# Performance work log

Measured on AMD Instinct MI355X. Metric: run time of the kernel, lower is better.

## Reference

```python
import jax, jax.numpy as jnp
import numpy as np

COUPLE_STRENGTH = 0.1
ITER_FISTA = 16
ITER_EIGENVAL = 20


def setup_inputs() -> dict:
    key = jax.random.key(0)
    k1, k2 = jax.random.split(key)
    # light field patches: (b, N, u, v, s, t, ch)
    x = jax.random.normal(k1, (8, 256, 5, 5, 4, 4, 3), dtype=jnp.float32)
    dim_signal = 5 * 5 * 4 * 4 * 3  # 1200
    dim_dict = 2 * dim_signal       # overcompleteness = 2 -> 2400
    D = jax.random.normal(k2, (dim_signal, dim_dict), dtype=jnp.float32)
    D = D / jnp.linalg.norm(D, axis=0, keepdims=True)  # UnitNorm(axis=0) constraint
    return {"x": x, "dictionary": D}


def _max_eigval(D):
    """von Mises power iteration for largest eigenvalue of D^T D."""
    v0 = jax.random.normal(jax.random.key(42), (D.shape[1],), dtype=D.dtype)
    v0 = v0 / jnp.linalg.norm(v0)

    def step(v, _):
        w = D.T @ (D @ v)
        n = jnp.linalg.norm(w)
        return w / n, n

    _, norms = jax.lax.scan(step, v0, None, length=ITER_EIGENVAL)
    return norms[-1]


def _soft_threshold(x, thr):
    return jnp.sign(x) * jnp.maximum(jnp.abs(x) - thr, 0.0)


def _sparse_code_fista(x2, D):
    """x2: (B, N, dim_signal); D: (dim_signal, dim_dict) -> codes (B, N, dim_dict)."""
    L = _max_eigval(D)            # Lipschitz constant of grad of 0.5*||Dz - x||^2
    thr = COUPLE_STRENGTH / L
    z0 = jnp.zeros(x2.shape[:-1] + (D.shape[1],), dtype=x2.dtype)
    carry0 = (z0, z0, jnp.float32(1.0))  # (z, y, t)

    def step(carry, _):
        z, y, t = carry
        recon = jnp.einsum('bnk,dk->bnd', y, D)             # (B,N,ds)
        grad = jnp.einsum('bnd,dk->bnk', recon - x2, D)     # (B,N,dd)
        z_new = _soft_threshold(y - grad / L, thr)
        t_new = 0.5 * (1.0 + jnp.sqrt(1.0 + 4.0 * t * t))
        y_new = z_new + ((t - 1.0) / t_new) * (z_new - z)   # Nesterov momentum
        return (z_new, y_new, t_new), None

    (z, _, _), _ = jax.lax.scan(step, carry0, None, length=ITER_FISTA)
    return z


def reference(x, dictionary):
    B, N, u, v, s, t, ch = x.shape
    x2 = x.reshape(B, N, u * v * s * t * ch)
    code = jax.lax.stop_gradient(_sparse_code_fista(x2, dictionary))
    recon = jnp.einsum('bnk,dk->bnd', code, dictionary)  # matmul(x, D, transpose_b=True)
    return recon.reshape(B, N, u, v, s, t, ch)
```

## Files before the change

### kernel.cpp

```cpp
#include <hip/hip_runtime.h>
#include <hip/hip_bf16.h>
#include <cmath>

#define DS 1200
#define DD 2400
#define MR 2048
#define KP 1216
#define NP1 1280
#define NG 2432
#define PPI 150

typedef __attribute__((ext_vector_type(8))) short s16x8;
typedef __attribute__((ext_vector_type(4))) float f32x4;

__device__ __forceinline__ float s2f(short s) {
    union { unsigned u; float f; } c;
    c.u = ((unsigned)(unsigned short)s) << 16;
    return c.f;
}
__device__ __forceinline__ short f2s(float f) {
    __hip_bfloat16 h = __float2bfloat16(f);
    return *reinterpret_cast<short*>(&h);
}


__device__ __forceinline__ unsigned rotl32(unsigned x, int d) {
    return (x << d) | (x >> (32 - d));
}

__device__ void threefry2x32(unsigned k0, unsigned k1, unsigned x0, unsigned x1,
                             unsigned* o0, unsigned* o1) {
    unsigned ks0 = k0, ks1 = k1, ks2 = k0 ^ k1 ^ 0x1BD11BDAu;
    const int rotA[4] = {13, 15, 26, 6};
    const int rotB[4] = {17, 29, 16, 24};
    x0 += ks0; x1 += ks1;
    #pragma unroll
    for (int r = 0; r < 4; r++) { x0 += x1; x1 = rotl32(x1, rotA[r]); x1 ^= x0; }
    x0 += ks1; x1 += ks2 + 1u;
    #pragma unroll
    for (int r = 0; r < 4; r++) { x0 += x1; x1 = rotl32(x1, rotB[r]); x1 ^= x0; }
    x0 += ks2; x1 += ks0 + 2u;
    #pragma unroll
    for (int r = 0; r < 4; r++) { x0 += x1; x1 = rotl32(x1, rotA[r]); x1 ^= x0; }
    x0 += ks0; x1 += ks1 + 3u;
    #pragma unroll
    for (int r = 0; r < 4; r++) { x0 += x1; x1 = rotl32(x1, rotB[r]); x1 ^= x0; }
    x0 += ks1; x1 += ks2 + 4u;
    #pragma unroll
    for (int r = 0; r < 4; r++) { x0 += x1; x1 = rotl32(x1, rotA[r]); x1 ^= x0; }
    x0 += ks2; x1 += ks0 + 5u;
    *o0 = x0; *o1 = x1;
}

__device__ float erfinv_f32(float x) {
    float w = -logf((1.0f - x) * (1.0f + x));
    float p;
    if (w < 5.0f) {
        w -= 2.5f;
        p = 2.81022636e-08f;
        p = fmaf(p, w, 3.43273939e-07f);
        p = fmaf(p, w, -3.5233877e-06f);
        p = fmaf(p, w, -4.39150654e-06f);
        p = fmaf(p, w, 0.00021858087f);
        p = fmaf(p, w, -0.00125372503f);
        p = fmaf(p, w, -0.00417768164f);
        p = fmaf(p, w, 0.246640727f);
        p = fmaf(p, w, 1.50140941f);
    } else {
        w = sqrtf(w) - 3.0f;
        p = -0.000200214257f;
        p = fmaf(p, w, 0.000100950558f);
        p = fmaf(p, w, 0.00134934322f);
        p = fmaf(p, w, -0.00367342844f);
        p = fmaf(p, w, 0.00573950773f);
        p = fmaf(p, w, -0.0076224613f);
        p = fmaf(p, w, 0.00943887047f);
        p = fmaf(p, w, 1.00167406f);
        p = fmaf(p, w, 2.83297682f);
    }
    return p * x;
}

__device__ float bits_to_normal(unsigned bits) {
    unsigned fb = (bits >> 9) | 0x3F800000u;
    float u01 = __uint_as_float(fb) - 1.0f;
    const float lo = -0.99999994f;
    float u = u01 * 2.0f + lo;
    u = fmaxf(lo, u);
    return 1.41421356237f * erfinv_f32(u);
}

__global__ void k_init(float* __restrict__ w0, float* __restrict__ w1,
                       float* __restrict__ part) {
    int tid = threadIdx.x;
    for (int i = tid; i < 21 * PPI; i += 256) part[i] = 0.0f;
    if (tid < 32) {
        w0[2400 + tid] = 0.0f;
        w1[2400 + tid] = 0.0f;
    }
    __shared__ float red[256];
    float local2 = 0.0f;
    for (int p = tid; p < DS; p += 256) {
        unsigned r0, r1;
        threefry2x32(0u, 42u, (unsigned)p, (unsigned)(DS + p), &r0, &r1);
        float n0 = bits_to_normal(r0);
        float n1 = bits_to_normal(r1);
        w0[p] = n0;
        w0[DS + p] = n1;
        local2 += n0 * n0 + n1 * n1;
    }
    red[tid] = local2;
    __syncthreads();
    for (int s = 128; s > 0; s >>= 1) {
        if (tid < s) red[tid] += red[tid + s];
        __syncthreads();
    }
    if (tid == 0) part[0] = red[0];
}

__global__ __launch_bounds__(1024) void k_gmv(const short* __restrict__ Grm,
                                              const float* __restrict__ win,
                                              const float* __restrict__ partin,
                                              float* __restrict__ wout,
                                              float* __restrict__ partout) {
    float s2 = 0.0f;
    for (int i = 0; i < PPI; i++) s2 += partin[i];
    float rn = 1.0f / sqrtf(s2);
    int wave = threadIdx.x >> 6, lane = threadIdx.x & 63;
    int row = blockIdx.x * 16 + wave;
    const s16x8* gh = (const s16x8*)(Grm + (size_t)row * NG);
    const float4* w4 = (const float4*)win;
    float acc = 0.0f;
    #pragma unroll
    for (int i = 0; i < 5; i++) {
        int c = lane + i * 64;
        if (c < 304) {
            s16x8 h = gh[c];
            float4 wa = w4[c * 2], wb = w4[c * 2 + 1];
            acc += s2f(h[0]) * wa.x + s2f(h[1]) * wa.y;
            acc += s2f(h[2]) * wa.z + s2f(h[3]) * wa.w;
            acc += s2f(h[4]) * wb.x + s2f(h[5]) * wb.y;
            acc += s2f(h[6]) * wb.z + s2f(h[7]) * wb.w;
        }
    }
    #pragma unroll
    for (int off = 32; off > 0; off >>= 1) acc += __shfl_xor(acc, off, 64);
    __shared__ float red[16];
    if (lane == 0) {
        float val = acc * rn;
        wout[row] = val;
        red[wave] = val * val;
    }
    __syncthreads();
    if (threadIdx.x == 0) {
        float s = 0.0f;
        #pragma unroll
        for (int i = 0; i < 16; i++) s += red[i];
        partout[blockIdx.x] = s;
    }
}

__global__ void k_fin(const float* __restrict__ part20, float* __restrict__ scal) {
    if (threadIdx.x == 0) {
        float s = 0.0f;
        for (int i = 0; i < PPI; i++) s += part20[i];
        float L = sqrtf(s);
        scal[0] = L;
        scal[1] = 1.0f / L;
        scal[2] = 0.1f / L;
    }
}

__global__ void k_makeD(const float* __restrict__ D, short* __restrict__ Dp) {
    int p = blockIdx.x * 256 + threadIdx.x;
    if (p >= NP1 * NG) return;
    int tile = p >> 10, win = p & 1023;
    int row = win >> 3, e = win & 7;
    int mt = tile / (NG >> 3), ct = tile % (NG >> 3);
    int d = mt * 128 + row, n = ct * 8 + e;
    float v = (d < DS && n < DD) ? D[(size_t)d * DD + n] : 0.0f;
    Dp[p] = f2s(v);
}

__global__ void k_makeX(const float* __restrict__ x, short* __restrict__ Xp) {
    int p = blockIdx.x * 256 + threadIdx.x;
    if (p >= MR * KP) return;
    int tile = p >> 10, win = p & 1023;
    int row = win >> 3, e = win & 7;
    int mt = tile / (KP >> 3), ct = tile % (KP >> 3);
    int m = mt * 128 + row, k = ct * 8 + e;
    float v = (k < DS) ? x[(size_t)m * DS + k] : 0.0f;
    Xp[p] = f2s(v);
}

__global__ void k_makeDt(const float* __restrict__ D,
                         short* __restrict__ Dthi, short* __restrict__ Dtlo) {
    __shared__ float t[32][33];
    int bc = blockIdx.x * 32;
    int bk = blockIdx.y * 32;
    int tx = threadIdx.x & 31, ty = threadIdx.x >> 5;
    for (int i = ty; i < 32; i += 8) {
        int k = bk + i, c = bc + tx;
        t[i][tx] = (k < DS && c < DD) ? D[(size_t)k * DD + c] : 0.0f;
    }
    __syncthreads();
    for (int i = ty; i < 32; i += 8) {
        int c = bc + i, k = bk + tx;
        float v = t[tx][i];
        short h = f2s(v);
        size_t po = ((size_t)(c >> 7) * (KP >> 3) + (k >> 3)) * 1024 +
                    ((c & 127) << 3) + (k & 7);
        Dthi[po] = h;
        Dtlo[po] = f2s(v - s2f(h));
    }
}

__global__ void k_makeW(const short* __restrict__ Grm, const float* __restrict__ scal,
                        short* __restrict__ Wp) {
    int i = blockIdx.x * 256 + threadIdx.x;
    if (i >= NG * NG / 8) return;
    float invL = scal[1];
    int e0 = i * 8;
    int band = e0 / (128 * NG);
    int rem = e0 - band * (128 * NG);
    int tile = rem >> 10;
    int row = (rem & 1023) >> 3;
    int m = band * 128 + row;
    int k0 = tile * 8;
    s16x8 g = *(const s16x8*)(Grm + (size_t)m * NG + k0);
    s16x8 wv;
    #pragma unroll
    for (int e = 0; e < 8; e++) {
        float wf = ((k0 + e == m) ? 1.0f : 0.0f) - s2f(g[e]) * invL;
        wv[e] = f2s(wf);
    }
    ((s16x8*)Wp)[i] = wv;
}

__global__ void k_fista0(const short* __restrict__ XDL, const float* __restrict__ scal,
                         short* __restrict__ Z, short* __restrict__ Y) {
    int i = blockIdx.x * 256 + threadIdx.x;
    if (i >= MR * NG / 8) return;
    float thr = scal[2];
    s16x8 xv = ((const s16x8*)XDL)[i];
    s16x8 zs;
    #pragma unroll
    for (int k = 0; k < 8; k++) {
        float gs = s2f(xv[k]);
        float az = fabsf(gs) - thr;
        float zn = (az > 0.0f) ? copysignf(az, gs) : 0.0f;
        zs[k] = f2s(zn);
    }
    ((s16x8*)Z)[i] = zs;
    ((s16x8*)Y)[i] = zs;
}

__device__ __forceinline__ void gload16(const void* g, void* l) {
    __builtin_amdgcn_global_load_lds(
        (const __attribute__((address_space(1))) unsigned int*)g,
        (__attribute__((address_space(3))) unsigned int*)l, 16, 0, 0);
}

template <int EPI, int SPLITM>
__global__ __launch_bounds__(256, 4) void mfma_gemm(
    const short* __restrict__ Ah, const short* __restrict__ Al, int CA,
    const short* __restrict__ Bh, const short* __restrict__ Bl, int CB,
    int K, int swz,
    const short* __restrict__ XDLp, const float* __restrict__ scal, float mom,
    short* __restrict__ Ynew, short* __restrict__ Zst,
    short* __restrict__ Grm,
    float* __restrict__ Out) {
    constexpr int ALO = 2048;
    constexpr int BHO = 4096;
    constexpr int BLO = 8192;
    constexpr int BUF = 12288;
    __shared__ __align__(16) short lds[2 * BUF];

    const int tid = threadIdx.x;
    const int w = tid >> 6, lane = tid & 63;
    const int fm = lane & 15, kg = lane >> 4;
    const int wr = w >> 1, wc = w & 1;

    int bx, by;
    if (swz) {
        int q = gridDim.x >> 3;
        int s = (blockIdx.x & 7) * q + (blockIdx.x >> 3);
        by = s & 31; bx = s >> 5;
    } else { bx = blockIdx.x; by = blockIdx.y; }
    const int m0 = by * 64, n0 = bx * 128;

    f32x4 acc[2][4];
    #pragma unroll
    for (int g = 0; g < 2; ++g)
        #pragma unroll
        for (int h = 0; h < 4; ++h) acc[g][h] = f32x4{0.f, 0.f, 0.f, 0.f};

    float invL = 0.0f, thr = 0.0f;
    if (EPI == 2 || EPI == 5) thr = scal[2];
    if (EPI == 3) invL = scal[1];

    const int half = (m0 >> 6) & 1;
    const int nk = K / (SPLITM ? 32 : 64);

    const size_t AbS = (size_t)(m0 & ~127) * CA + w * 1024 + half * 512 + lane * 8;
    const size_t BbS = (size_t)n0 * CB + w * 512 + lane * 8;
    const size_t AbN = (size_t)(m0 & ~127) * CA + half * 512 + lane * 8;
    const size_t BbN = (size_t)n0 * CB + lane * 8;

    auto STAGE = [&](int t, int cur) {
        short* bp = &lds[cur * BUF];
        if constexpr (SPLITM == 1) {
            const size_t kk = (size_t)t << 12;
            gload16(Ah + AbS + kk, bp + w * 512);
            gload16(Bh + BbS + kk, bp + BHO + w * 512);
            gload16(Bh + BbS + kk + 2048, bp + BHO + 2048 + w * 512);
            gload16(Al + AbS + kk, bp + ALO + w * 512);
            gload16(Bl + BbS + kk, bp + BLO + w * 512);
            gload16(Bl + BbS + kk + 2048, bp + BLO + 2048 + w * 512);
        } else if constexpr (SPLITM == 2) {
            const size_t kk = (size_t)t << 12;
            gload16(Ah + AbS + kk, bp + w * 512);
            gload16(Bh + BbS + kk, bp + BHO + w * 512);
            gload16(Bh + BbS + kk + 2048, bp + BHO + 2048 + w * 512);
            gload16(Bl + BbS + kk, bp + BLO + w * 512);
            gload16(Bl + BbS + kk + 2048, bp + BLO + 2048 + w * 512);
        } else {
            const size_t kk = (size_t)t << 13;
            const int cs0 = 2 * w, cs1 = 2 * w + 1;
            gload16(Ah + AbN + kk + cs0 * 1024, bp + cs0 * 512);
            gload16(Ah + AbN + kk + cs1 * 1024, bp + cs1 * 512);
            gload16(Bh + BbN + kk + cs0 * 1024,       bp + BHO + cs0 * 1024);
            gload16(Bh + BbN + kk + cs0 * 1024 + 512, bp + BHO + cs0 * 1024 + 512);
            gload16(Bh + BbN + kk + cs1 * 1024,       bp + BHO + cs1 * 1024);
            gload16(Bh + BbN + kk + cs1 * 1024 + 512, bp + BHO + cs1 * 1024 + 512);
        }
    };

    STAGE(0, 0);

    for (int t = 0; t < nk; ++t) {
        __syncthreads();
        if (t + 1 < nk) STAGE(t + 1, (t + 1) & 1);
        const short* bs = &lds[(t & 1) * BUF];

        #pragma unroll
        for (int ks = 0; ks < (SPLITM ? 1 : 2); ++ks) {
            const int c = ks * 4 + kg;
            s16x8 a[2], b[4];
            #pragma unroll
            for (int g = 0; g < 2; ++g)
                a[g] = *(const s16x8*)&bs[c * 512 + (wr * 32 + g * 16 + fm) * 8];
            #pragma unroll
            for (int h = 0; h < 4; ++h)
                b[h] = *(const s16x8*)&bs[BHO + c * 1024 + (wc * 64 + h * 16 + fm) * 8];
            if constexpr (SPLITM == 1) {
                s16x8 a2[2], b2[4];
                #pragma unroll
                for (int g = 0; g < 2; ++g)
                    a2[g] = *(const s16x8*)&bs[ALO + c * 512 + (wr * 32 + g * 16 + fm) * 8];
                #pragma unroll
                for (int h = 0; h < 4; ++h)
                    b2[h] = *(const s16x8*)&bs[BLO + c * 1024 + (wc * 64 + h * 16 + fm) * 8];
                #pragma unroll
                for (int g = 0; g < 2; ++g)
                    #pragma unroll
                    for (int h = 0; h < 4; ++h) {
                        acc[g][h] = __builtin_amdgcn_mfma_f32_16x16x32_bf16(a[g], b[h], acc[g][h], 0, 0, 0);
                        acc[g][h] = __builtin_amdgcn_mfma_f32_16x16x32_bf16(a[g], b2[h], acc[g][h], 0, 0, 0);
                        acc[g][h] = __builtin_amdgcn_mfma_f32_16x16x32_bf16(a2[g], b[h], acc[g][h], 0, 0, 0);
                    }
            } else if constexpr (SPLITM == 2) {
                s16x8 b2[4];
                #pragma unroll
                for (int h = 0; h < 4; ++h)
                    b2[h] = *(const s16x8*)&bs[BLO + c * 1024 + (wc * 64 + h * 16 + fm) * 8];
                #pragma unroll
                for (int g = 0; g < 2; ++g)
                    #pragma unroll
                    for (int h = 0; h < 4; ++h) {
                        acc[g][h] = __builtin_amdgcn_mfma_f32_16x16x32_bf16(a[g], b[h], acc[g][h], 0, 0, 0);
                        acc[g][h] = __builtin_amdgcn_mfma_f32_16x16x32_bf16(a[g], b2[h], acc[g][h], 0, 0, 0);
                    }
            } else {
                #pragma unroll
                for (int g = 0; g < 2; ++g)
                    #pragma unroll
                    for (int h = 0; h < 4; ++h)
                        acc[g][h] = __builtin_amdgcn_mfma_f32_16x16x32_bf16(a[g], b[h], acc[g][h], 0, 0, 0);
            }
        }
    }

    #pragma unroll
    for (int g = 0; g < 2; ++g) {
        #pragma unroll
        for (int h = 0; h < 4; ++h) {
            #pragma unroll
            for (int j = 0; j < 4; ++j) {
                int m = m0 + wr * 32 + g * 16 + kg * 4 + j;
                int n = n0 + wc * 64 + h * 16 + fm;
                float v = acc[g][h][j];
                if (EPI == 0) {
                    if (n < DS) Out[(size_t)m * DS + n] = v;
                } else if (EPI == 2) {
                    size_t pz = (size_t)(m & ~127) * NG + ((n >> 3) << 10) +
                                ((m & 127) << 3) + (n & 7);
                    float gs = v + s2f(XDLp[pz]);
                    float az = fabsf(gs) - thr;
                    float zn = (az > 0.0f) ? copysignf(az, gs) : 0.0f;
                    float zold = s2f(Zst[pz]);
                    float yn = zn + mom * (zn - zold);
                    Zst[pz] = f2s(zn);
                    Ynew[pz] = f2s(yn);
                } else if (EPI == 5) {
                    size_t pz = (size_t)(m & ~127) * NG + ((n >> 3) << 10) +
                                ((m & 127) << 3) + (n & 7);
                    float gs = v + s2f(XDLp[pz]);
                    float az = fabsf(gs) - thr;
                    float zn = (az > 0.0f) ? copysignf(az, gs) : 0.0f;
                    Zst[pz] = f2s(zn);
                } else if (EPI == 3) {
                    size_t pz = (size_t)(m & ~127) * NG + ((n >> 3) << 10) +
                                ((m & 127) << 3) + (n & 7);
                    Ynew[pz] = f2s(v * invL);
                } else {
                    Grm[(size_t)m * NG + n] = f2s(v);
                }
            }
        }
    }
}

extern "C" void kernel_launch(void* const* d_in, const int* in_sizes, int n_in,
                              void* d_out, int out_size, void* d_ws, size_t ws_size,
                              hipStream_t stream) {
    const float* x = (const float*)d_in[0];
    const float* D = (const float*)d_in[1];
    float* out = (float*)d_out;

    char* wsb = (char*)d_ws;
    float* w0 = (float*)wsb;
    float* w1 = w0 + 2432;
    float* part = w1 + 2432;
    float* scal = part + 3200;

    char* p = wsb + 65536;
    short* Dp   = (short*)p; p += (size_t)NP1 * NG * 2;
    short* Dthi = (short*)p; p += (size_t)NG * KP * 2;
    short* Dtlo = (short*)p; p += (size_t)NG * KP * 2;
    short* Xp   = (short*)p; p += (size_t)MR * KP * 2;
    short* Wp   = (short*)p; p += (size_t)NG * NG * 2;
    short* Grm  = (short*)p; p += (size_t)NG * NG * 2;
    short* XDLp = (short*)p; p += (size_t)MR * NG * 2;
    short* Ya   = (short*)p; p += (size_t)MR * NG * 2;
    short* Yb   = (short*)p; p += (size_t)MR * NG * 2;
    short* Zp   = (short*)p; p += (size_t)MR * NG * 2;

    k_makeD<<<(NP1 * NG + 255) / 256, 256, 0, stream>>>(D, Dp);
    k_makeDt<<<dim3(NG / 32, KP / 32), 256, 0, stream>>>(D, Dthi, Dtlo);
    k_makeX<<<(MR * KP + 255) / 256, 256, 0, stream>>>(x, Xp);

    mfma_gemm<4, 1><<<dim3(NG / 128, NG / 64), 256, 0, stream>>>(
        Dthi, Dtlo, KP, Dthi, Dtlo, KP, KP, 0,
        nullptr, nullptr, 0.0f, nullptr, nullptr, Grm, nullptr);

    k_init<<<1, 256, 0, stream>>>(w0, w1, part);
    for (int j = 0; j < 20; j++) {
        const float* win = (j & 1) ? w1 : w0;
        float* wout = (j & 1) ? w0 : w1;
        k_gmv<<<PPI, 1024, 0, stream>>>(Grm, win, part + j * PPI, wout,
                                        part + (j + 1) * PPI);
    }
    k_fin<<<1, 64, 0, stream>>>(part + 20 * PPI, scal);

    k_makeW<<<(NG * NG / 8 + 255) / 256, 256, 0, stream>>>(Grm, scal, Wp);

    mfma_gemm<3, 2><<<dim3(608), 256, 0, stream>>>(
        Xp, nullptr, KP, Dthi, Dtlo, KP, KP, 1,
        nullptr, scal, 0.0f, XDLp, nullptr, nullptr, nullptr);

    k_fista0<<<(MR * NG / 8 + 255) / 256, 256, 0, stream>>>(XDLp, scal, Zp, Ya);

    float t = 1.6180339887f;
    for (int i = 1; i < 15; i++) {
        float tn = 0.5f * (1.0f + sqrtf(1.0f + 4.0f * t * t));
        float mom = (t - 1.0f) / tn;
        t = tn;
        short* Yc = (i & 1) ? Ya : Yb;
        short* Yn = (i & 1) ? Yb : Ya;
        mfma_gemm<2, 0><<<dim3(608), 256, 0, stream>>>(
            Yc, nullptr, NG, Wp, nullptr, NG, NG, 1,
            XDLp, scal, mom, Yn, Zp, nullptr, nullptr);
    }
    {
        short* Yc = Ya;
        mfma_gemm<5, 0><<<dim3(608), 256, 0, stream>>>(
            Yc, nullptr, NG, Wp, nullptr, NG, NG, 1,
            XDLp, scal, 0.0f, nullptr, Zp, nullptr, nullptr);
    }

    mfma_gemm<0, 0><<<dim3(320), 256, 0, stream>>>(
        Zp, nullptr, NG, Dp, nullptr, NG, NG, 1,
        nullptr, nullptr, 0.0f, nullptr, nullptr, nullptr, out);
}
```

Measured before the change: 857.7 us.

## Add dedicated FISTA GEMM kernel loading A directly to registers

```diff
diff --git a/kernel.cpp b/kernel.cpp
--- a/kernel.cpp
+++ b/kernel.cpp
@@ -261,13 +261,144 @@
         (__attribute__((address_space(3))) unsigned int*)l, 16, 0, 0);
 }
 
+__global__ __launch_bounds__(256, 4) void fista_gemm(
+    const short* __restrict__ Yp, const short* __restrict__ Wq,
+    const short* __restrict__ XDLp, const float* __restrict__ scal, float mom,
+    short* __restrict__ Ynew, short* __restrict__ Zst, int lastIter) {
+    __shared__ __align__(16) short ldsB[2][8192];
+
+    const int tid = threadIdx.x;
+    const int w = tid >> 6, lane = tid & 63;
+    const int fm = lane & 15, kg = lane >> 4;
+    const int wr = w >> 1, wc = w & 1;
+
+    const int q = 76;
+    const int s = (blockIdx.x & 7) * q + (blockIdx.x >> 3);
+    const int by = s & 31, bx = s >> 5;
+    const int m0 = by * 64, n0 = bx * 128;
+
+    f32x4 acc[2][4];
+    #pragma unroll
+    for (int g = 0; g < 2; ++g)
+        #pragma unroll
+        for (int h = 0; h < 4; ++h) acc[g][h] = f32x4{0.f, 0.f, 0.f, 0.f};
+
+    const float thr = scal[2];
+
+    const int band = m0 & ~127, half = (m0 >> 6) & 1;
+    const int mloc = half * 64 + wr * 32 + fm;
+    const short* Ab = Yp + (size_t)band * NG + mloc * 8 + kg * 1024;
+    const short* Bb = Wq + (size_t)n0 * NG + tid * 8;
+
+    s16x8 A0_0, A0_1, A0_2, A0_3;
+    s16x8 A1_0, A1_1, A1_2, A1_3;
+
+#define LOADA(st, r0, r1, r2, r3)                           \
+    {                                                       \
+        const short* p_ = Ab + (size_t)(st) * 8192;         \
+        r0 = *(const s16x8*)(p_);                           \
+        r1 = *(const s16x8*)(p_ + 128);                     \
+        r2 = *(const s16x8*)(p_ + 4096);                    \
+        r3 = *(const s16x8*)(p_ + 4224);                    \
+    }
+#define STAGEB(st, buf)                                     \
+    {                                                       \
+        const short* q_ = Bb + (size_t)(st) * 8192;         \
+        short* bp_ = &ldsB[buf][0];                         \
+        gload16(q_,        bp_ + w * 512);                  \
+        gload16(q_ + 2048, bp_ + 2048 + w * 512);           \
+        gload16(q_ + 4096, bp_ + 4096 + w * 512);           \
+        gload16(q_ + 6144, bp_ + 6144 + w * 512);           \
+    }
+#define COMP(buf, r0, r1, r2, r3)                                              \
+    {                                                                          \
+        const short* bs_ = &ldsB[buf][0];                                      \
+        {                                                                      \
+            const int c_ = kg;                                                 \
+            s16x8 b0 = *(const s16x8*)&bs_[c_ * 1024 + (wc * 64 + 0 * 16 + fm) * 8];  \
+            s16x8 b1 = *(const s16x8*)&bs_[c_ * 1024 + (wc * 64 + 1 * 16 + fm) * 8];  \
+            s16x8 b2 = *(const s16x8*)&bs_[c_ * 1024 + (wc * 64 + 2 * 16 + fm) * 8];  \
+            s16x8 b3 = *(const s16x8*)&bs_[c_ * 1024 + (wc * 64 + 3 * 16 + fm) * 8];  \
+            acc[0][0] = __builtin_amdgcn_mfma_f32_16x16x32_bf16(r0, b0, acc[0][0], 0, 0, 0); \
+            acc[0][1] = __builtin_amdgcn_mfma_f32_16x16x32_bf16(r0, b1, acc[0][1], 0, 0, 0); \
+            acc[0][2] = __builtin_amdgcn_mfma_f32_16x16x32_bf16(r0, b2, acc[0][2], 0, 0, 0); \
+            acc[0][3] = __builtin_amdgcn_mfma_f32_16x16x32_bf16(r0, b3, acc[0][3], 0, 0, 0); \
+            acc[1][0] = __builtin_amdgcn_mfma_f32_16x16x32_bf16(r1, b0, acc[1][0], 0, 0, 0); \
+            acc[1][1] = __builtin_amdgcn_mfma_f32_16x16x32_bf16(r1, b1, acc[1][1], 0, 0, 0); \
+            acc[1][2] = __builtin_amdgcn_mfma_f32_16x16x32_bf16(r1, b2, acc[1][2], 0, 0, 0); \
+            acc[1][3] = __builtin_amdgcn_mfma_f32_16x16x32_bf16(r1, b3, acc[1][3], 0, 0, 0); \
+        }                                                                      \
+        {                                                                      \
+            const int c_ = 4 + kg;                                             \
+            s16x8 b0 = *(const s16x8*)&bs_[c_ * 1024 + (wc * 64 + 0 * 16 + fm) * 8];  \
+            s16x8 b1 = *(const s16x8*)&bs_[c_ * 1024 + (wc * 64 + 1 * 16 + fm) * 8];  \
+            s16x8 b2 = *(const s16x8*)&bs_[c_ * 1024 + (wc * 64 + 2 * 16 + fm) * 8];  \
+            s16x8 b3 = *(const s16x8*)&bs_[c_ * 1024 + (wc * 64 + 3 * 16 + fm) * 8];  \
+            acc[0][0] = __builtin_amdgcn_mfma_f32_16x16x32_bf16(r2, b0, acc[0][0], 0, 0, 0); \
+            acc[0][1] = __builtin_amdgcn_mfma_f32_16x16x32_bf16(r2, b1, acc[0][1], 0, 0, 0); \
+            acc[0][2] = __builtin_amdgcn_mfma_f32_16x16x32_bf16(r2, b2, acc[0][2], 0, 0, 0); \
+            acc[0][3] = __builtin_amdgcn_mfma_f32_16x16x32_bf16(r2, b3, acc[0][3], 0, 0, 0); \
+            acc[1][0] = __builtin_amdgcn_mfma_f32_16x16x32_bf16(r3, b0, acc[1][0], 0, 0, 0); \
+            acc[1][1] = __builtin_amdgcn_mfma_f32_16x16x32_bf16(r3, b1, acc[1][1], 0, 0, 0); \
+            acc[1][2] = __builtin_amdgcn_mfma_f32_16x16x32_bf16(r3, b2, acc[1][2], 0, 0, 0); \
+            acc[1][3] = __builtin_amdgcn_mfma_f32_16x16x32_bf16(r3, b3, acc[1][3], 0, 0, 0); \
+        }                                                                      \
+    }
+
+    LOADA(0, A0_0, A0_1, A0_2, A0_3);
+    STAGEB(0, 0);
+
+    for (int t = 0; t < 38; t += 2) {
+        __syncthreads();
+        STAGEB(t + 1, 1);
+        LOADA(t + 1, A1_0, A1_1, A1_2, A1_3);
+        COMP(0, A0_0, A0_1, A0_2, A0_3);
+        __syncthreads();
+        if (t + 2 < 38) {
+            STAGEB(t + 2, 0);
+            LOADA(t + 2, A0_0, A0_1, A0_2, A0_3);
+        }
+        COMP(1, A1_0, A1_1, A1_2, A1_3);
+    }
+
+#undef LOADA
+#undef STAGEB
+#undef COMP
+
+    #pragma unroll
+    for (int g = 0; g < 2; ++g) {
+        #pragma unroll
+        for (int h = 0; h < 4; ++h) {
+            #pragma unroll
+            for (int j = 0; j < 4; ++j) {
+                int m = m0 + wr * 32 + g * 16 + kg * 4 + j;
+                int n = n0 + wc * 64 + h * 16 + fm;
+                float v = acc[g][h][j];
+                size_t pz = (size_t)(m & ~127) * NG + ((n >> 3) << 10) +
+                            ((m & 127) << 3) + (n & 7);
+                float gs = v + s2f(XDLp[pz]);
+                float az = fabsf(gs) - thr;
+                float zn = (az > 0.0f) ? copysignf(az, gs) : 0.0f;
+                if (!lastIter) {
+                    float zold = s2f(Zst[pz]);
+                    float yn = zn + mom * (zn - zold);
+                    Zst[pz] = f2s(zn);
+                    Ynew[pz] = f2s(yn);
+                } else {
+                    Zst[pz] = f2s(zn);
+                }
+            }
+        }
+    }
+}
+
 template <int EPI, int SPLITM>
 __global__ __launch_bounds__(256, 4) void mfma_gemm(
     const short* __restrict__ Ah, const short* __restrict__ Al, int CA,
     const short* __restrict__ Bh, const short* __restrict__ Bl, int CB,
     int K, int swz,
-    const short* __restrict__ XDLp, const float* __restrict__ scal, float mom,
-    short* __restrict__ Ynew, short* __restrict__ Zst,
+    const float* __restrict__ scal,
+    short* __restrict__ Ynew,
     short* __restrict__ Grm,
     float* __restrict__ Out) {
     constexpr int ALO = 2048;
@@ -295,8 +426,7 @@
         #pragma unroll
         for (int h = 0; h < 4; ++h) acc[g][h] = f32x4{0.f, 0.f, 0.f, 0.f};
 
-    float invL = 0.0f, thr = 0.0f;
-    if (EPI == 2 || EPI == 5) thr = scal[2];
+    float invL = 0.0f;
     if (EPI == 3) invL = scal[1];
 
     const int half = (m0 >> 6) & 1;
@@ -402,23 +532,6 @@
                 float v = acc[g][h][j];
                 if (EPI == 0) {
                     if (n < DS) Out[(size_t)m * DS + n] = v;
-                } else if (EPI == 2) {
-                    size_t pz = (size_t)(m & ~127) * NG + ((n >> 3) << 10) +
-                                ((m & 127) << 3) + (n & 7);
-                    float gs = v + s2f(XDLp[pz]);
-                    float az = fabsf(gs) - thr;
-                    float zn = (az > 0.0f) ? copysignf(az, gs) : 0.0f;
-                    float zold = s2f(Zst[pz]);
-                    float yn = zn + mom * (zn - zold);
-                    Zst[pz] = f2s(zn);
-                    Ynew[pz] = f2s(yn);
-                } else if (EPI == 5) {
-                    size_t pz = (size_t)(m & ~127) * NG + ((n >> 3) << 10) +
-                                ((m & 127) << 3) + (n & 7);
-                    float gs = v + s2f(XDLp[pz]);
-                    float az = fabsf(gs) - thr;
-                    float zn = (az > 0.0f) ? copysignf(az, gs) : 0.0f;
-                    Zst[pz] = f2s(zn);
                 } else if (EPI == 3) {
                     size_t pz = (size_t)(m & ~127) * NG + ((n >> 3) << 10) +
                                 ((m & 127) << 3) + (n & 7);
@@ -462,7 +575,7 @@
 
     mfma_gemm<4, 1><<<dim3(NG / 128, NG / 64), 256, 0, stream>>>(
         Dthi, Dtlo, KP, Dthi, Dtlo, KP, KP, 0,
-        nullptr, nullptr, 0.0f, nullptr, nullptr, Grm, nullptr);
+        nullptr, nullptr, Grm, nullptr);
 
     k_init<<<1, 256, 0, stream>>>(w0, w1, part);
     for (int j = 0; j < 20; j++) {
@@ -477,7 +590,7 @@
 
     mfma_gemm<3, 2><<<dim3(608), 256, 0, stream>>>(
         Xp, nullptr, KP, Dthi, Dtlo, KP, KP, 1,
-        nullptr, scal, 0.0f, XDLp, nullptr, nullptr, nullptr);
+        scal, XDLp, nullptr, nullptr);
 
     k_fista0<<<(MR * NG / 8 + 255) / 256, 256, 0, stream>>>(XDLp, scal, Zp, Ya);
 
@@ -488,18 +601,13 @@
         t = tn;
         short* Yc = (i & 1) ? Ya : Yb;
         short* Yn = (i & 1) ? Yb : Ya;
-        mfma_gemm<2, 0><<<dim3(608), 256, 0, stream>>>(
-            Yc, nullptr, NG, Wp, nullptr, NG, NG, 1,
-            XDLp, scal, mom, Yn, Zp, nullptr, nullptr);
-    }
-    {
-        short* Yc = Ya;
-        mfma_gemm<5, 0><<<dim3(608), 256, 0, stream>>>(
-            Yc, nullptr, NG, Wp, nullptr, NG, NG, 1,
-            XDLp, scal, 0.0f, nullptr, Zp, nullptr, nullptr);
-    }
+        fista_gemm<<<dim3(608), 256, 0, stream>>>(
+            Yc, Wp, XDLp, scal, mom, Yn, Zp, 0);
+    }
+    fista_gemm<<<dim3(608), 256, 0, stream>>>(
+        Ya, Wp, XDLp, scal, 0.0f, nullptr, Zp, 1);
 
     mfma_gemm<0, 0><<<dim3(320), 256, 0, stream>>>(
         Zp, nullptr, NG, Dp, nullptr, NG, NG, 1,
-        nullptr, nullptr, 0.0f, nullptr, nullptr, nullptr, out);
-}
+        nullptr, nullptr, nullptr, out);
+}
```

Result: slower. 1.136 ms (+32.4%).
